# Optimization experiments

Hardware: AMD Instinct MI355X
Metric: run time of the kernel (lower is better)

## Reference

```python
import jax, jax.numpy as jnp
import numpy as np

B, D, H, FPL, L, LOG2_T = 65536, 768, 512, 4, 16, 19
T = 2 ** LOG2_T
BASE_RES, FINEST_RES = 16, 512
PRIMES = jnp.array([1, 2654435761, 805459861], dtype=jnp.uint32)


def setup_inputs() -> dict:
    key = jax.random.key(0)
    ks = jax.random.split(key, 8)
    t = jax.random.uniform(ks[0], (B,), dtype=jnp.float32)
    x = jax.random.normal(ks[1], (B, D), dtype=jnp.float32)
    cond = jax.random.uniform(ks[2], (B, 2), dtype=jnp.float32)
    # one embedding table per level, Instant-NGP init U(-1e-4, 1e-4)
    tables = jax.random.uniform(ks[3], (L, T, FPL), dtype=jnp.float32,
                                minval=-1e-4, maxval=1e-4)
    in_dim = D + L * FPL  # 832

    def lin(k, fan_in, fan_out):
        return jax.random.normal(k, (fan_in, fan_out), dtype=jnp.float32) / np.sqrt(fan_in).astype(np.float32)

    W0, b0 = lin(ks[4], in_dim, H), jnp.zeros((H,), jnp.float32)
    W1, b1 = lin(ks[5], H, H), jnp.zeros((H,), jnp.float32)
    W2, b2 = lin(ks[6], H, H), jnp.zeros((H,), jnp.float32)
    W3, b3 = lin(ks[7], H, D), jnp.zeros((D,), jnp.float32)
    return dict(t=t, x=x, cond=cond, tables=tables,
                W0=W0, b0=b0, W1=W1, b1=b1, W2=W2, b2=b2, W3=W3, b3=b3)


def hash_encode(coords, tables):
    """coords: [B,3] in [0,1]; tables: [L,T,F] -> [B, L*F]."""
    Ln, Tn, Fn = tables.shape
    growth = np.exp((np.log(FINEST_RES) - np.log(BASE_RES)) / (Ln - 1))
    scales = jnp.asarray(np.floor(BASE_RES * growth ** np.arange(Ln)),
                         dtype=coords.dtype)                      # [L]
    xf = coords[:, None, :] * scales[None, :, None]               # [B,L,3]
    xl = jnp.floor(xf)
    w = xf - xl                                                   # [B,L,3] trilinear frac
    xi = xl.astype(jnp.uint32)
    # 8 cube-corner offsets
    offs = jnp.asarray(np.stack(np.meshgrid([0, 1], [0, 1], [0, 1],
                                            indexing='ij'), -1).reshape(8, 3),
                       dtype=jnp.uint32)                          # [8,3]
    corners = xi[:, :, None, :] + offs[None, None]                # [B,L,8,3]
    h = corners * PRIMES                                          # uint32 wraparound hash
    idx = (h[..., 0] ^ h[..., 1] ^ h[..., 2]) & jnp.uint32(Tn - 1)  # [B,L,8]
    feats = tables[jnp.arange(Ln)[None, :, None], idx]            # [B,L,8,F] gather
    offs_f = offs.astype(coords.dtype)
    wc = jnp.prod(jnp.where(offs_f[None, None] == 1,
                            w[:, :, None, :], 1 - w[:, :, None, :]), axis=-1)  # [B,L,8]
    out = jnp.einsum('blc,blcf->blf', wc, feats)                  # [B,L,F]
    return out.reshape(out.shape[0], Ln * Fn)


def reference(t, x, cond, tables, W0, b0, W1, b1, W2, b2, W3, b3):
    tcol = t[:, None] if t.ndim == 1 else t
    params3 = jnp.concatenate([cond, tcol], axis=-1)   # [B,3]
    enc = hash_encode(params3, tables)                  # [B,64]
    h = jnp.concatenate([x, enc], axis=-1)              # [B,832]
    h = jax.nn.silu(h @ W0 + b0)
    h = jax.nn.silu(h @ W1 + b1)
    h = jax.nn.silu(h @ W2 + b2)
    return h @ W3 + b3                                  # [B,768]
```

## Files before the change

### kernel.cpp

```cpp
#include <hip/hip_runtime.h>
#include <hip/hip_bf16.h>
#include <math.h>


#define T_SIZE 524288
#define T_MASK (T_SIZE - 1)

typedef _Float16 f16;
typedef _Float16 f16x8 __attribute__((ext_vector_type(8)));
typedef _Float16 f16x4 __attribute__((ext_vector_type(4)));
typedef float f32x4 __attribute__((ext_vector_type(4)));

struct Scales { float s[16]; };

__global__ void wfrag(const float* __restrict__ W, f16* __restrict__ Wf, int K, int N) {
  int tid = blockIdx.x * 256 + threadIdx.x;
  int lane = tid & 63, frag = tid >> 6;
  int KS = K >> 5;
  int nblk = frag / KS, ks = frag - nblk * KS;
  if (nblk * 16 >= N) return;
  int n = nblk * 16 + (lane & 15);
  int kb = ks * 32 + (lane >> 4) * 8;
  f16x8 v;
#pragma unroll
  for (int j = 0; j < 8; ++j) v[j] = (f16)W[(size_t)(kb + j) * N + n];
  *(f16x8*)(Wf + (size_t)frag * 512 + lane * 8) = v;
}

__device__ __forceinline__ float silu_f(float v) {
  return v * __builtin_amdgcn_rcpf(1.f + __expf(-v));
}

__device__ __forceinline__ f16x8 cvt8(f32x4 a, f32x4 b) {
  return (f16x8){ (f16)a.x, (f16)a.y, (f16)a.z, (f16)a.w,
                  (f16)b.x, (f16)b.y, (f16)b.z, (f16)b.w };
}

template<int NF, int KSTEPS>
__device__ __forceinline__ void kloop_dp(
    const f16* __restrict__ actS, const f16* __restrict__ Wf, int fragRow0,
    int l16, int lhi, int lane, f32x4 (&acc)[4][4]) {
#pragma unroll
  for (int mi = 0; mi < 4; ++mi)
#pragma unroll
    for (int ni = 0; ni < NF; ++ni) acc[mi][ni] = (f32x4){0.f, 0.f, 0.f, 0.f};

  f16x8 bfU[NF], bfV[NF];
  const f16* wbase = Wf + ((size_t)fragRow0 * KSTEPS) * 512 + lane * 8;
#pragma unroll
  for (int ni = 0; ni < NF; ++ni)
    bfU[ni] = *(const f16x8*)(wbase + (size_t)(ni * KSTEPS + 0) * 512);
#pragma unroll
  for (int ni = 0; ni < NF; ++ni)
    bfV[ni] = *(const f16x8*)(wbase + (size_t)(ni * KSTEPS + 1) * 512);

#pragma unroll 1
  for (int ks = 0; ks < KSTEPS; ks += 2) {
    f16x8 af[4];
#pragma unroll
    for (int mi = 0; mi < 4; ++mi) {
      int r = mi * 16 + l16;
      af[mi] = *(const f16x8*)(actS + r * 512 + ((ks * 32 + lhi * 8) ^ ((r & 7) << 3)));
    }
#pragma unroll
    for (int mi = 0; mi < 4; ++mi)
#pragma unroll
      for (int ni = 0; ni < NF; ++ni)
        acc[mi][ni] = __builtin_amdgcn_mfma_f32_16x16x32_f16(bfU[ni], af[mi], acc[mi][ni], 0, 0, 0);
    if (ks + 2 < KSTEPS) {
#pragma unroll
      for (int ni = 0; ni < NF; ++ni)
        bfU[ni] = *(const f16x8*)(wbase + (size_t)(ni * KSTEPS + ks + 2) * 512);
    }
#pragma unroll
    for (int mi = 0; mi < 4; ++mi) {
      int r = mi * 16 + l16;
      af[mi] = *(const f16x8*)(actS + r * 512 + (((ks + 1) * 32 + lhi * 8) ^ ((r & 7) << 3)));
    }
#pragma unroll
    for (int mi = 0; mi < 4; ++mi)
#pragma unroll
      for (int ni = 0; ni < NF; ++ni)
        acc[mi][ni] = __builtin_amdgcn_mfma_f32_16x16x32_f16(bfV[ni], af[mi], acc[mi][ni], 0, 0, 0);
    if (ks + 3 < KSTEPS) {
#pragma unroll
      for (int ni = 0; ni < NF; ++ni)
        bfV[ni] = *(const f16x8*)(wbase + (size_t)(ni * KSTEPS + ks + 3) * 512);
    }
  }
}

__global__ __launch_bounds__(512, 4) void fused_mlp(
    const float* __restrict__ x, const float* __restrict__ t,
    const float* __restrict__ cond, const float* __restrict__ tables,
    const f16* __restrict__ Wf0, const f16* __restrict__ Wf1,
    const f16* __restrict__ Wf2, const f16* __restrict__ Wf3,
    const float* __restrict__ b0, const float* __restrict__ b1,
    const float* __restrict__ b2, const float* __restrict__ b3,
    float* __restrict__ outp, Scales scl) {
  __shared__ f16 act[64 * 512];
  f16* stg = act;
#define STG(p, kk) (stg + (p) * 5120 + (kk) * 2560)

  const int tid = threadIdx.x;
  const int wave = tid >> 6, lane = tid & 63;
  const int l16 = lane & 15, lhi = lane >> 4;
  const int rowBase = blockIdx.x * 64;
  const int sr = tid >> 3, c8 = tid & 7;
  const int skk = c8 >> 2, sco = (c8 & 3) * 8;

  f16x8 er;
  {
    int row = rowBase + sr;
    float c0 = cond[2 * row], c1 = cond[2 * row + 1], c2 = t[row];
    unsigned idx[2][8];
    float    wcw[2][8];
#pragma unroll
    for (int d = 0; d < 2; ++d) {
      int l = c8 * 2 + d;
      float s = scl.s[l];
      float xf0 = c0 * s, xf1 = c1 * s, xf2 = c2 * s;
      float xl0 = floorf(xf0), xl1 = floorf(xf1), xl2 = floorf(xf2);
      float w0 = xf0 - xl0, w1 = xf1 - xl1, w2 = xf2 - xl2;
      unsigned xi0 = (unsigned)xl0, xi1 = (unsigned)xl1, xi2 = (unsigned)xl2;
      unsigned h0 = xi0, h1 = xi1 * 2654435761u, h2 = xi2 * 805459861u;
      unsigned g0 = xi0 + 1u, g1 = (xi1 + 1u) * 2654435761u, g2 = (xi2 + 1u) * 805459861u;
#pragma unroll
      for (int c = 0; c < 8; ++c) {
        unsigned ax = (c >> 2) & 1u, ay = (c >> 1) & 1u, az = c & 1u;
        unsigned hh = (ax ? g0 : h0) ^ (ay ? g1 : h1) ^ (az ? g2 : h2);
        idx[d][c] = hh & T_MASK;
        wcw[d][c] = (ax ? w0 : 1.f - w0) * (ay ? w1 : 1.f - w1) * (az ? w2 : 1.f - w2);
      }
    }
    const f32x4* tl0 = (const f32x4*)tables + (size_t)(c8 * 2) * T_SIZE;
    f32x4 fv[2][8];
#pragma unroll
    for (int d = 0; d < 2; ++d)
#pragma unroll
      for (int c = 0; c < 8; ++c)
        fv[d][c] = tl0[(size_t)d * T_SIZE + idx[d][c]];
#pragma unroll
    for (int d = 0; d < 2; ++d) {
      float a0 = 0.f, a1 = 0.f, a2 = 0.f, a3 = 0.f;
#pragma unroll
      for (int c = 0; c < 8; ++c) {
        a0 += wcw[d][c] * fv[d][c].x; a1 += wcw[d][c] * fv[d][c].y;
        a2 += wcw[d][c] * fv[d][c].z; a3 += wcw[d][c] * fv[d][c].w;
      }
      er[d * 4 + 0] = (f16)a0; er[d * 4 + 1] = (f16)a1;
      er[d * 4 + 2] = (f16)a2; er[d * 4 + 3] = (f16)a3;
    }
  }

  f32x4 acc[4][4];
#pragma unroll
  for (int mi = 0; mi < 4; ++mi)
#pragma unroll
    for (int ni = 0; ni < 4; ++ni) acc[mi][ni] = (f32x4){0.f, 0.f, 0.f, 0.f};

  {
    const float* xrow = x + (size_t)(rowBase + sr) * 768 + c8 * 8;
    {
      f32x4 a = __builtin_nontemporal_load((const f32x4*)(xrow));
      f32x4 b = __builtin_nontemporal_load((const f32x4*)(xrow + 4));
      *(f16x8*)(STG(0, skk) + sr * 40 + sco) = cvt8(a, b);
    }
    f32x4 pA0 = __builtin_nontemporal_load((const f32x4*)(xrow + 64));
    f32x4 pA1 = __builtin_nontemporal_load((const f32x4*)(xrow + 68));
    f32x4 pB0, pB1;
    const f16* wb = Wf0 + lane * 8;
    __syncthreads();

#pragma unroll 1
    for (int ks = 0; ks < 13; ++ks) {
      if (ks + 2 < 12) {
        pB0 = __builtin_nontemporal_load((const f32x4*)(xrow + (ks + 2) * 64));
        pB1 = __builtin_nontemporal_load((const f32x4*)(xrow + (ks + 2) * 64 + 4));
      }
      f16x8 bf[2][4];
#pragma unroll
      for (int kk = 0; kk < 2; ++kk)
#pragma unroll
        for (int ni = 0; ni < 4; ++ni)
          bf[kk][ni] = *(const f16x8*)(wb + (size_t)((wave * 4 + ni) * 26 + 2 * ks + kk) * 512);

      const f16* rb = stg + (ks & 1) * 5120;
#pragma unroll
      for (int kk = 0; kk < 2; ++kk)
#pragma unroll
        for (int mi = 0; mi < 4; ++mi) {
          f16x8 af = *(const f16x8*)(rb + kk * 2560 + (mi * 16 + l16) * 40 + lhi * 8);
#pragma unroll
          for (int ni = 0; ni < 4; ++ni)
            acc[mi][ni] = __builtin_amdgcn_mfma_f32_16x16x32_f16(bf[kk][ni], af, acc[mi][ni], 0, 0, 0);
        }

      if (ks < 11) {
        *(f16x8*)(STG((ks + 1) & 1, skk) + sr * 40 + sco) = cvt8(pA0, pA1);
        pA0 = pB0; pA1 = pB1;
      } else if (ks == 11) {
        *(f16x8*)(STG(0, skk) + sr * 40 + sco) = er;
      }
      __syncthreads();
    }
  }

  auto epi_act = [&](const float* __restrict__ bias) {
    __syncthreads();
#pragma unroll
    for (int mi = 0; mi < 4; ++mi) {
      const int row = mi * 16 + l16;
#pragma unroll
      for (int ni = 0; ni < 4; ++ni) {
        const int col = wave * 64 + ni * 16 + lhi * 4;
        float4 bv = *(const float4*)(bias + col);
        f16x4 o;
        o[0] = (f16)silu_f(acc[mi][ni][0] + bv.x);
        o[1] = (f16)silu_f(acc[mi][ni][1] + bv.y);
        o[2] = (f16)silu_f(acc[mi][ni][2] + bv.z);
        o[3] = (f16)silu_f(acc[mi][ni][3] + bv.w);
        *(f16x4*)(act + row * 512 + (col ^ ((row & 7) << 3))) = o;
      }
    }
    __syncthreads();
  };
  epi_act(b0);

  kloop_dp<4, 16>(act, Wf1, wave * 4, l16, lhi, lane, acc); epi_act(b1);
  kloop_dp<4, 16>(act, Wf2, wave * 4, l16, lhi, lane, acc); epi_act(b2);

  kloop_dp<4, 16>(act, Wf3, wave * 4, l16, lhi, lane, acc);
#pragma unroll
  for (int mi = 0; mi < 4; ++mi) {
    const size_t row = (size_t)(rowBase + mi * 16 + l16);
#pragma unroll
    for (int ni = 0; ni < 4; ++ni) {
      const int col = wave * 64 + ni * 16 + lhi * 4;
      float4 bv = *(const float4*)(b3 + col);
      f32x4 o = { acc[mi][ni][0] + bv.x, acc[mi][ni][1] + bv.y,
                  acc[mi][ni][2] + bv.z, acc[mi][ni][3] + bv.w };
      __builtin_nontemporal_store(o, (f32x4*)(outp + row * 768 + col));
    }
  }

  kloop_dp<2, 16>(act, Wf3, 32 + wave * 2, l16, lhi, lane, acc);
#pragma unroll
  for (int mi = 0; mi < 4; ++mi) {
    const size_t row = (size_t)(rowBase + mi * 16 + l16);
#pragma unroll
    for (int ni = 0; ni < 2; ++ni) {
      const int col = 512 + wave * 32 + ni * 16 + lhi * 4;
      float4 bv = *(const float4*)(b3 + col);
      f32x4 o = { acc[mi][ni][0] + bv.x, acc[mi][ni][1] + bv.y,
                  acc[mi][ni][2] + bv.z, acc[mi][ni][3] + bv.w };
      __builtin_nontemporal_store(o, (f32x4*)(outp + row * 768 + col));
    }
  }
#undef STG
}

extern "C" void kernel_launch(void* const* d_in, const int* in_sizes, int n_in,
                              void* d_out, int out_size, void* d_ws, size_t ws_size,
                              hipStream_t stream) {
  const float* t    = (const float*)d_in[0];
  const float* x    = (const float*)d_in[1];
  const float* cond = (const float*)d_in[2];
  const float* tab  = (const float*)d_in[3];
  const float* W0   = (const float*)d_in[4];
  const float* b0   = (const float*)d_in[5];
  const float* W1   = (const float*)d_in[6];
  const float* b1   = (const float*)d_in[7];
  const float* W2   = (const float*)d_in[8];
  const float* b2   = (const float*)d_in[9];
  const float* W3   = (const float*)d_in[10];
  const float* b3   = (const float*)d_in[11];
  float* out = (float*)d_out;
  (void)in_sizes; (void)n_in; (void)out_size; (void)ws_size;

  char* ws = (char*)d_ws;
  f16* Wf0 = (f16*)(ws + 0);
  f16* Wf1 = (f16*)(ws + 851968);
  f16* Wf2 = (f16*)(ws + 1376256);
  f16* Wf3 = (f16*)(ws + 1900544);

  wfrag<<<dim3(208), 256, 0, stream>>>(W0, Wf0, 832, 512);
  wfrag<<<dim3(128), 256, 0, stream>>>(W1, Wf1, 512, 512);
  wfrag<<<dim3(128), 256, 0, stream>>>(W2, Wf2, 512, 512);
  wfrag<<<dim3(192), 256, 0, stream>>>(W3, Wf3, 512, 768);

  Scales sc;
  {
    double growth = exp((log(512.0) - log(16.0)) / 15.0);
    for (int l = 0; l < 16; ++l) sc.s[l] = (float)floor(16.0 * pow(growth, (double)l));
  }

  fused_mlp<<<dim3(1024), 512, 0, stream>>>(x, t, cond, tab, Wf0, Wf1, Wf2, Wf3,
                                            b0, b1, b2, b3, out, sc);
}
```

Before: 291.4 us.

## Split input prep into separate kernel and use 128-row blocks with direct LDS loads

Moves hash encoding and the fp32-to-fp16 conversion of x into a separate prep kernel that writes an f16 [B,832] buffer to workspace. The MLP kernel now uses 1024-thread blocks covering 128 rows, so each weight fragment loaded from global serves twice as many rows, and it streams layer-0 inputs with global_load_lds into swizzled double buffers. This adds an extra HBM round trip for the intermediate activations and a second launch, and a 128 KB LDS block limits occupancy to one block per CU.

```diff
diff --git a/kernel.cpp b/kernel.cpp
--- a/kernel.cpp
+++ b/kernel.cpp
@@ -12,6 +12,10 @@
 typedef float f32x4 __attribute__((ext_vector_type(4)));
 
 struct Scales { float s[16]; };
+
+#define GLD16(gsrc, ldst) __builtin_amdgcn_global_load_lds( \
+    (const __attribute__((address_space(1))) void*)(gsrc),  \
+    (__attribute__((address_space(3))) void*)(ldst), 16, 0, 0)
 
 __global__ void wfrag(const float* __restrict__ W, f16* __restrict__ Wf, int K, int N) {
   int tid = blockIdx.x * 256 + threadIdx.x;
@@ -36,82 +40,16 @@
                   (f16)b.x, (f16)b.y, (f16)b.z, (f16)b.w };
 }
 
-template<int NF, int KSTEPS>
-__device__ __forceinline__ void kloop_dp(
-    const f16* __restrict__ actS, const f16* __restrict__ Wf, int fragRow0,
-    int l16, int lhi, int lane, f32x4 (&acc)[4][4]) {
-#pragma unroll
-  for (int mi = 0; mi < 4; ++mi)
-#pragma unroll
-    for (int ni = 0; ni < NF; ++ni) acc[mi][ni] = (f32x4){0.f, 0.f, 0.f, 0.f};
-
-  f16x8 bfU[NF], bfV[NF];
-  const f16* wbase = Wf + ((size_t)fragRow0 * KSTEPS) * 512 + lane * 8;
-#pragma unroll
-  for (int ni = 0; ni < NF; ++ni)
-    bfU[ni] = *(const f16x8*)(wbase + (size_t)(ni * KSTEPS + 0) * 512);
-#pragma unroll
-  for (int ni = 0; ni < NF; ++ni)
-    bfV[ni] = *(const f16x8*)(wbase + (size_t)(ni * KSTEPS + 1) * 512);
-
-#pragma unroll 1
-  for (int ks = 0; ks < KSTEPS; ks += 2) {
-    f16x8 af[4];
-#pragma unroll
-    for (int mi = 0; mi < 4; ++mi) {
-      int r = mi * 16 + l16;
-      af[mi] = *(const f16x8*)(actS + r * 512 + ((ks * 32 + lhi * 8) ^ ((r & 7) << 3)));
-    }
-#pragma unroll
-    for (int mi = 0; mi < 4; ++mi)
-#pragma unroll
-      for (int ni = 0; ni < NF; ++ni)
-        acc[mi][ni] = __builtin_amdgcn_mfma_f32_16x16x32_f16(bfU[ni], af[mi], acc[mi][ni], 0, 0, 0);
-    if (ks + 2 < KSTEPS) {
-#pragma unroll
-      for (int ni = 0; ni < NF; ++ni)
-        bfU[ni] = *(const f16x8*)(wbase + (size_t)(ni * KSTEPS + ks + 2) * 512);
-    }
-#pragma unroll
-    for (int mi = 0; mi < 4; ++mi) {
-      int r = mi * 16 + l16;
-      af[mi] = *(const f16x8*)(actS + r * 512 + (((ks + 1) * 32 + lhi * 8) ^ ((r & 7) << 3)));
-    }
-#pragma unroll
-    for (int mi = 0; mi < 4; ++mi)
-#pragma unroll
-      for (int ni = 0; ni < NF; ++ni)
-        acc[mi][ni] = __builtin_amdgcn_mfma_f32_16x16x32_f16(bfV[ni], af[mi], acc[mi][ni], 0, 0, 0);
-    if (ks + 3 < KSTEPS) {
-#pragma unroll
-      for (int ni = 0; ni < NF; ++ni)
-        bfV[ni] = *(const f16x8*)(wbase + (size_t)(ni * KSTEPS + ks + 3) * 512);
-    }
-  }
-}
-
-__global__ __launch_bounds__(512, 4) void fused_mlp(
+__global__ __launch_bounds__(256) void prep(
     const float* __restrict__ x, const float* __restrict__ t,
     const float* __restrict__ cond, const float* __restrict__ tables,
-    const f16* __restrict__ Wf0, const f16* __restrict__ Wf1,
-    const f16* __restrict__ Wf2, const f16* __restrict__ Wf3,
-    const float* __restrict__ b0, const float* __restrict__ b1,
-    const float* __restrict__ b2, const float* __restrict__ b3,
-    float* __restrict__ outp, Scales scl) {
-  __shared__ f16 act[64 * 512];
-  f16* stg = act;
-#define STG(p, kk) (stg + (p) * 5120 + (kk) * 2560)
-
-  const int tid = threadIdx.x;
-  const int wave = tid >> 6, lane = tid & 63;
-  const int l16 = lane & 15, lhi = lane >> 4;
-  const int rowBase = blockIdx.x * 64;
-  const int sr = tid >> 3, c8 = tid & 7;
-  const int skk = c8 >> 2, sco = (c8 & 3) * 8;
-
-  f16x8 er;
+    f16* __restrict__ H0, Scales scl) {
+  const int row = blockIdx.x * 32 + (threadIdx.x >> 3);
+  const int c8 = threadIdx.x & 7;
+  const float* xr = x + (size_t)row * 768;
+  f16* hr = H0 + (size_t)row * 832;
+
   {
-    int row = rowBase + sr;
     float c0 = cond[2 * row], c1 = cond[2 * row + 1], c2 = t[row];
     unsigned idx[2][8];
     float    wcw[2][8];
@@ -140,6 +78,7 @@
 #pragma unroll
       for (int c = 0; c < 8; ++c)
         fv[d][c] = tl0[(size_t)d * T_SIZE + idx[d][c]];
+    f16x8 er;
 #pragma unroll
     for (int d = 0; d < 2; ++d) {
       float a0 = 0.f, a1 = 0.f, a2 = 0.f, a3 = 0.f;
@@ -151,7 +90,92 @@
       er[d * 4 + 0] = (f16)a0; er[d * 4 + 1] = (f16)a1;
       er[d * 4 + 2] = (f16)a2; er[d * 4 + 3] = (f16)a3;
     }
-  }
+    *(f16x8*)(hr + 768 + c8 * 8) = er;
+  }
+
+#pragma unroll
+  for (int j = 0; j < 12; ++j) {
+    int col = j * 64 + c8 * 8;
+    f32x4 a = __builtin_nontemporal_load((const f32x4*)(xr + col));
+    f32x4 b = __builtin_nontemporal_load((const f32x4*)(xr + col + 4));
+    *(f16x8*)(hr + col) = cvt8(a, b);
+  }
+}
+
+template<int NF, int KSTEPS>
+__device__ __forceinline__ void kloop_dp(
+    const f16* __restrict__ actS, const f16* __restrict__ Wf, int fragRow0,
+    int l16, int lhi, int lane, f32x4 (&acc)[4][4]) {
+#pragma unroll
+  for (int mi = 0; mi < 4; ++mi)
+#pragma unroll
+    for (int ni = 0; ni < NF; ++ni) acc[mi][ni] = (f32x4){0.f, 0.f, 0.f, 0.f};
+
+  f16x8 bfU[NF], bfV[NF];
+  const f16* wbase = Wf + ((size_t)fragRow0 * KSTEPS) * 512 + lane * 8;
+#pragma unroll
+  for (int ni = 0; ni < NF; ++ni)
+    bfU[ni] = *(const f16x8*)(wbase + (size_t)(ni * KSTEPS + 0) * 512);
+#pragma unroll
+  for (int ni = 0; ni < NF; ++ni)
+    bfV[ni] = *(const f16x8*)(wbase + (size_t)(ni * KSTEPS + 1) * 512);
+
+#pragma unroll 1
+  for (int ks = 0; ks < KSTEPS; ks += 2) {
+    f16x8 af[4];
+#pragma unroll
+    for (int mi = 0; mi < 4; ++mi) {
+      int r = mi * 16 + l16;
+      af[mi] = *(const f16x8*)(actS + r * 512 + ((ks * 32 + lhi * 8) ^ ((r & 7) << 3)));
+    }
+#pragma unroll
+    for (int mi = 0; mi < 4; ++mi)
+#pragma unroll
+      for (int ni = 0; ni < NF; ++ni)
+        acc[mi][ni] = __builtin_amdgcn_mfma_f32_16x16x32_f16(bfU[ni], af[mi], acc[mi][ni], 0, 0, 0);
+    if (ks + 2 < KSTEPS) {
+#pragma unroll
+      for (int ni = 0; ni < NF; ++ni)
+        bfU[ni] = *(const f16x8*)(wbase + (size_t)(ni * KSTEPS + ks + 2) * 512);
+    }
+#pragma unroll
+    for (int mi = 0; mi < 4; ++mi) {
+      int r = mi * 16 + l16;
+      af[mi] = *(const f16x8*)(actS + r * 512 + (((ks + 1) * 32 + lhi * 8) ^ ((r & 7) << 3)));
+    }
+#pragma unroll
+    for (int mi = 0; mi < 4; ++mi)
+#pragma unroll
+      for (int ni = 0; ni < NF; ++ni)
+        acc[mi][ni] = __builtin_amdgcn_mfma_f32_16x16x32_f16(bfV[ni], af[mi], acc[mi][ni], 0, 0, 0);
+    if (ks + 3 < KSTEPS) {
+#pragma unroll
+      for (int ni = 0; ni < NF; ++ni)
+        bfV[ni] = *(const f16x8*)(wbase + (size_t)(ni * KSTEPS + ks + 3) * 512);
+    }
+  }
+}
+
+__global__ __launch_bounds__(1024, 4) void fused_mlp(
+    const f16* __restrict__ H0,
+    const f16* __restrict__ Wf0, const f16* __restrict__ Wf1,
+    const f16* __restrict__ Wf2, const f16* __restrict__ Wf3,
+    const float* __restrict__ b0, const float* __restrict__ b1,
+    const float* __restrict__ b2, const float* __restrict__ b3,
+    float* __restrict__ outp) {
+  __shared__ f16 act[128 * 512];
+  f16* stg = act;
+
+  const int tid = threadIdx.x;
+  const int wave = tid >> 6, lane = tid & 63;
+  const int l16 = lane & 15, lhi = lane >> 4;
+  const int wr = wave >> 3, wc = wave & 7;
+  const int rowBase = blockIdx.x * 128;
+  const int r = tid >> 3, c8 = tid & 7;
+
+  const f16* h0r = H0 + (size_t)(rowBase + r) * 832 + (size_t)((c8 ^ (r & 7)) * 8);
+  f16* ldsA = stg + wave * 512;
+  f16* ldsB = stg + 8192 + wave * 512;
 
   f32x4 acc[4][4];
 #pragma unroll
@@ -160,48 +184,28 @@
     for (int ni = 0; ni < 4; ++ni) acc[mi][ni] = (f32x4){0.f, 0.f, 0.f, 0.f};
 
   {
-    const float* xrow = x + (size_t)(rowBase + sr) * 768 + c8 * 8;
-    {
-      f32x4 a = __builtin_nontemporal_load((const f32x4*)(xrow));
-      f32x4 b = __builtin_nontemporal_load((const f32x4*)(xrow + 4));
-      *(f16x8*)(STG(0, skk) + sr * 40 + sco) = cvt8(a, b);
-    }
-    f32x4 pA0 = __builtin_nontemporal_load((const f32x4*)(xrow + 64));
-    f32x4 pA1 = __builtin_nontemporal_load((const f32x4*)(xrow + 68));
-    f32x4 pB0, pB1;
-    const f16* wb = Wf0 + lane * 8;
+    GLD16(h0r, ldsA);
     __syncthreads();
-
 #pragma unroll 1
     for (int ks = 0; ks < 13; ++ks) {
-      if (ks + 2 < 12) {
-        pB0 = __builtin_nontemporal_load((const f32x4*)(xrow + (ks + 2) * 64));
-        pB1 = __builtin_nontemporal_load((const f32x4*)(xrow + (ks + 2) * 64 + 4));
-      }
+      if (ks < 12) GLD16(h0r + (ks + 1) * 64, (ks & 1) ? ldsA : ldsB);
       f16x8 bf[2][4];
 #pragma unroll
       for (int kk = 0; kk < 2; ++kk)
 #pragma unroll
         for (int ni = 0; ni < 4; ++ni)
-          bf[kk][ni] = *(const f16x8*)(wb + (size_t)((wave * 4 + ni) * 26 + 2 * ks + kk) * 512);
-
-      const f16* rb = stg + (ks & 1) * 5120;
+          bf[kk][ni] = *(const f16x8*)(Wf0 + (size_t)((wc * 4 + ni) * 26 + ks * 2 + kk) * 512 + lane * 8);
+      const f16* rb = stg + (ks & 1) * 8192 + wr * 4096;
 #pragma unroll
       for (int kk = 0; kk < 2; ++kk)
 #pragma unroll
         for (int mi = 0; mi < 4; ++mi) {
-          f16x8 af = *(const f16x8*)(rb + kk * 2560 + (mi * 16 + l16) * 40 + lhi * 8);
+          int r2 = mi * 16 + l16;
+          f16x8 af = *(const f16x8*)(rb + r2 * 64 + (((kk * 4 + lhi) ^ (r2 & 7)) << 3));
 #pragma unroll
           for (int ni = 0; ni < 4; ++ni)
             acc[mi][ni] = __builtin_amdgcn_mfma_f32_16x16x32_f16(bf[kk][ni], af, acc[mi][ni], 0, 0, 0);
         }
-
-      if (ks < 11) {
-        *(f16x8*)(STG((ks + 1) & 1, skk) + sr * 40 + sco) = cvt8(pA0, pA1);
-        pA0 = pB0; pA1 = pB1;
-      } else if (ks == 11) {
-        *(f16x8*)(STG(0, skk) + sr * 40 + sco) = er;
-      }
       __syncthreads();
     }
   }
@@ -210,10 +214,10 @@
     __syncthreads();
 #pragma unroll
     for (int mi = 0; mi < 4; ++mi) {
-      const int row = mi * 16 + l16;
+      const int row = wr * 64 + mi * 16 + l16;
 #pragma unroll
       for (int ni = 0; ni < 4; ++ni) {
-        const int col = wave * 64 + ni * 16 + lhi * 4;
+        const int col = wc * 64 + ni * 16 + lhi * 4;
         float4 bv = *(const float4*)(bias + col);
         f16x4 o;
         o[0] = (f16)silu_f(acc[mi][ni][0] + bv.x);
@@ -227,16 +231,18 @@
   };
   epi_act(b0);
 
-  kloop_dp<4, 16>(act, Wf1, wave * 4, l16, lhi, lane, acc); epi_act(b1);
-  kloop_dp<4, 16>(act, Wf2, wave * 4, l16, lhi, lane, acc); epi_act(b2);
-
-  kloop_dp<4, 16>(act, Wf3, wave * 4, l16, lhi, lane, acc);
+  const f16* actW = act + wr * 64 * 512;
+
+  kloop_dp<4, 16>(actW, Wf1, wc * 4, l16, lhi, lane, acc); epi_act(b1);
+  kloop_dp<4, 16>(actW, Wf2, wc * 4, l16, lhi, lane, acc); epi_act(b2);
+
+  kloop_dp<4, 16>(actW, Wf3, wc * 4, l16, lhi, lane, acc);
 #pragma unroll
   for (int mi = 0; mi < 4; ++mi) {
-    const size_t row = (size_t)(rowBase + mi * 16 + l16);
+    const size_t row = (size_t)(rowBase + wr * 64 + mi * 16 + l16);
 #pragma unroll
     for (int ni = 0; ni < 4; ++ni) {
-      const int col = wave * 64 + ni * 16 + lhi * 4;
+      const int col = wc * 64 + ni * 16 + lhi * 4;
       float4 bv = *(const float4*)(b3 + col);
       f32x4 o = { acc[mi][ni][0] + bv.x, acc[mi][ni][1] + bv.y,
                   acc[mi][ni][2] + bv.z, acc[mi][ni][3] + bv.w };
@@ -244,20 +250,19 @@
     }
   }
 
-  kloop_dp<2, 16>(act, Wf3, 32 + wave * 2, l16, lhi, lane, acc);
+  kloop_dp<2, 16>(actW, Wf3, 32 + wc * 2, l16, lhi, lane, acc);
 #pragma unroll
   for (int mi = 0; mi < 4; ++mi) {
-    const size_t row = (size_t)(rowBase + mi * 16 + l16);
+    const size_t row = (size_t)(rowBase + wr * 64 + mi * 16 + l16);
 #pragma unroll
     for (int ni = 0; ni < 2; ++ni) {
-      const int col = 512 + wave * 32 + ni * 16 + lhi * 4;
+      const int col = 512 + wc * 32 + ni * 16 + lhi * 4;
       float4 bv = *(const float4*)(b3 + col);
       f32x4 o = { acc[mi][ni][0] + bv.x, acc[mi][ni][1] + bv.y,
                   acc[mi][ni][2] + bv.z, acc[mi][ni][3] + bv.w };
       __builtin_nontemporal_store(o, (f32x4*)(outp + row * 768 + col));
     }
   }
-#undef STG
 }
 
 extern "C" void kernel_launch(void* const* d_in, const int* in_sizes, int n_in,
@@ -283,6 +288,7 @@
   f16* Wf1 = (f16*)(ws + 851968);
   f16* Wf2 = (f16*)(ws + 1376256);
   f16* Wf3 = (f16*)(ws + 1900544);
+  f16* H0  = (f16*)(ws + 2686976);
 
   wfrag<<<dim3(208), 256, 0, stream>>>(W0, Wf0, 832, 512);
   wfrag<<<dim3(128), 256, 0, stream>>>(W1, Wf1, 512, 512);
@@ -295,6 +301,8 @@
     for (int l = 0; l < 16; ++l) sc.s[l] = (float)floor(16.0 * pow(growth, (double)l));
   }
 
-  fused_mlp<<<dim3(1024), 512, 0, stream>>>(x, t, cond, tab, Wf0, Wf1, Wf2, Wf3,
-                                            b0, b1, b2, b3, out, sc);
-}
+  prep<<<dim3(2048), 256, 0, stream>>>(x, t, cond, tab, H0, sc);
+
+  fused_mlp<<<dim3(512), 1024, 0, stream>>>(H0, Wf0, Wf1, Wf2, Wf3,
+                                            b0, b1, b2, b3, out);
+}
```

Result: slower. 348.3 us (+19.5%).

## Stream x tiles into LDS via async global_load_lds with triple buffering

Applied to the files above, without the earlier changes.

Layer 0 now loads fp32 x tiles straight into LDS with global_load_lds (16-byte) into a triple-buffered, XOR-swizzled staging area, and converts to fp16 when reading the MFMA operands. The per-iteration __syncthreads is replaced by explicit vmcnt waits plus s_barrier, with raised wave priority around the MFMA block. The hash encoding result gets its own small LDS buffer and is consumed in a separate final k-step. The aim is to drop the register round-trip and the per-step store/sync for x staging and to overlap loads better. The cost is extra LDS (fp32 staging, more buffers), which may reduce occupancy, and it relies on hand-tuned waitcnt values.

```diff
diff --git a/kernel.cpp b/kernel.cpp
--- a/kernel.cpp
+++ b/kernel.cpp
@@ -12,6 +12,11 @@
 typedef float f32x4 __attribute__((ext_vector_type(4)));
 
 struct Scales { float s[16]; };
+
+#define GLD16(gsrc, ldst) __builtin_amdgcn_global_load_lds( \
+    (const __attribute__((address_space(1))) void*)(gsrc),  \
+    (__attribute__((address_space(3))) void*)(ldst), 16, 0, 0)
+#define SB() __builtin_amdgcn_sched_barrier(0)
 
 __global__ void wfrag(const float* __restrict__ W, f16* __restrict__ Wf, int K, int N) {
   int tid = blockIdx.x * 256 + threadIdx.x;
@@ -99,17 +104,15 @@
     const float* __restrict__ b2, const float* __restrict__ b3,
     float* __restrict__ outp, Scales scl) {
   __shared__ f16 act[64 * 512];
-  f16* stg = act;
-#define STG(p, kk) (stg + (p) * 5120 + (kk) * 2560)
+  __shared__ f16 encs[64 * 64];
+  char* stg = (char*)act;
 
   const int tid = threadIdx.x;
   const int wave = tid >> 6, lane = tid & 63;
   const int l16 = lane & 15, lhi = lane >> 4;
   const int rowBase = blockIdx.x * 64;
   const int sr = tid >> 3, c8 = tid & 7;
-  const int skk = c8 >> 2, sco = (c8 & 3) * 8;
-
-  f16x8 er;
+
   {
     int row = rowBase + sr;
     float c0 = cond[2 * row], c1 = cond[2 * row + 1], c2 = t[row];
@@ -140,6 +143,7 @@
 #pragma unroll
       for (int c = 0; c < 8; ++c)
         fv[d][c] = tl0[(size_t)d * T_SIZE + idx[d][c]];
+    f16x8 er;
 #pragma unroll
     for (int d = 0; d < 2; ++d) {
       float a0 = 0.f, a1 = 0.f, a2 = 0.f, a3 = 0.f;
@@ -151,6 +155,7 @@
       er[d * 4 + 0] = (f16)a0; er[d * 4 + 1] = (f16)a1;
       er[d * 4 + 2] = (f16)a2; er[d * 4 + 3] = (f16)a3;
     }
+    *(f16x8*)(encs + sr * 64 + ((c8 ^ (sr & 7)) * 8)) = er;
   }
 
   f32x4 acc[4][4];
@@ -160,49 +165,70 @@
     for (int ni = 0; ni < 4; ++ni) acc[mi][ni] = (f32x4){0.f, 0.f, 0.f, 0.f};
 
   {
-    const float* xrow = x + (size_t)(rowBase + sr) * 768 + c8 * 8;
-    {
-      f32x4 a = __builtin_nontemporal_load((const f32x4*)(xrow));
-      f32x4 b = __builtin_nontemporal_load((const f32x4*)(xrow + 4));
-      *(f16x8*)(STG(0, skk) + sr * 40 + sco) = cvt8(a, b);
-    }
-    f32x4 pA0 = __builtin_nontemporal_load((const f32x4*)(xrow + 64));
-    f32x4 pA1 = __builtin_nontemporal_load((const f32x4*)(xrow + 68));
-    f32x4 pB0, pB1;
-    const f16* wb = Wf0 + lane * 8;
+    const float* xsrc = x + (size_t)(rowBase + sr) * 768 + (size_t)((c8 ^ (sr & 7)) * 4);
+
+    GLD16(xsrc,      stg + wave * 1024);
+    GLD16(xsrc + 32, stg + 8192 + wave * 1024);
     __syncthreads();
 
+    int pr = 0, pw = 1;
 #pragma unroll 1
-    for (int ks = 0; ks < 13; ++ks) {
-      if (ks + 2 < 12) {
-        pB0 = __builtin_nontemporal_load((const f32x4*)(xrow + (ks + 2) * 64));
-        pB1 = __builtin_nontemporal_load((const f32x4*)(xrow + (ks + 2) * 64 + 4));
+    for (int s = 0; s < 12; ++s) {
+      if (s < 11) {
+        GLD16(xsrc + (s + 1) * 64,      stg + pw * 16384 + wave * 1024);
+        GLD16(xsrc + (s + 1) * 64 + 32, stg + pw * 16384 + 8192 + wave * 1024);
       }
+      SB();
       f16x8 bf[2][4];
 #pragma unroll
       for (int kk = 0; kk < 2; ++kk)
 #pragma unroll
         for (int ni = 0; ni < 4; ++ni)
-          bf[kk][ni] = *(const f16x8*)(wb + (size_t)((wave * 4 + ni) * 26 + 2 * ks + kk) * 512);
-
-      const f16* rb = stg + (ks & 1) * 5120;
+          bf[kk][ni] = *(const f16x8*)(Wf0 + (size_t)((wave * 4 + ni) * 26 + 2 * s + kk) * 512 + lane * 8);
+      SB();
+      if (s < 11) asm volatile("s_waitcnt vmcnt(10)" ::: "memory");
+      else        asm volatile("s_waitcnt vmcnt(8)"  ::: "memory");
+      SB();
+      __builtin_amdgcn_s_barrier();
+      SB();
+      const char* rb = stg + pr * 16384;
+      __builtin_amdgcn_s_setprio(1);
 #pragma unroll
       for (int kk = 0; kk < 2; ++kk)
 #pragma unroll
         for (int mi = 0; mi < 4; ++mi) {
-          f16x8 af = *(const f16x8*)(rb + kk * 2560 + (mi * 16 + l16) * 40 + lhi * 8);
+          int r2 = mi * 16 + l16;
+          const char* rowb = rb + kk * 8192 + r2 * 128;
+          f32x4 a = *(const f32x4*)(rowb + (((lhi * 2)     ^ (r2 & 7)) << 4));
+          f32x4 b = *(const f32x4*)(rowb + (((lhi * 2 + 1) ^ (r2 & 7)) << 4));
+          f16x8 af = cvt8(a, b);
 #pragma unroll
           for (int ni = 0; ni < 4; ++ni)
             acc[mi][ni] = __builtin_amdgcn_mfma_f32_16x16x32_f16(bf[kk][ni], af, acc[mi][ni], 0, 0, 0);
         }
-
-      if (ks < 11) {
-        *(f16x8*)(STG((ks + 1) & 1, skk) + sr * 40 + sco) = cvt8(pA0, pA1);
-        pA0 = pB0; pA1 = pB1;
-      } else if (ks == 11) {
-        *(f16x8*)(STG(0, skk) + sr * 40 + sco) = er;
-      }
-      __syncthreads();
+      __builtin_amdgcn_s_setprio(0);
+      SB();
+      pr = (pr == 2) ? 0 : pr + 1;
+      pw = (pw == 2) ? 0 : pw + 1;
+    }
+
+    {
+      f16x8 bf[2][4];
+#pragma unroll
+      for (int kk = 0; kk < 2; ++kk)
+#pragma unroll
+        for (int ni = 0; ni < 4; ++ni)
+          bf[kk][ni] = *(const f16x8*)(Wf0 + (size_t)((wave * 4 + ni) * 26 + 24 + kk) * 512 + lane * 8);
+#pragma unroll
+      for (int kk = 0; kk < 2; ++kk)
+#pragma unroll
+        for (int mi = 0; mi < 4; ++mi) {
+          int r2 = mi * 16 + l16;
+          f16x8 af = *(const f16x8*)(encs + r2 * 64 + (((kk * 4 + lhi) ^ (r2 & 7)) * 8));
+#pragma unroll
+          for (int ni = 0; ni < 4; ++ni)
+            acc[mi][ni] = __builtin_amdgcn_mfma_f32_16x16x32_f16(bf[kk][ni], af, acc[mi][ni], 0, 0, 0);
+        }
     }
   }
 
@@ -257,7 +283,6 @@
       __builtin_nontemporal_store(o, (f32x4*)(outp + row * 768 + col));
     }
   }
-#undef STG
 }
 
 extern "C" void kernel_launch(void* const* d_in, const int* in_sizes, int n_in,
```

Result: slower. 299.2 us (+2.7%).

## Split hash encoding and x conversion into a prep kernel writing MFMA fragments

Applied to the files above, without the earlier changes.

Moves the hash-grid encoding and the fp32-to-fp16 conversion of x out of the fused MLP into a separate prep kernel. That kernel writes the layer-0 input directly in MFMA fragment layout to workspace. The first layer then reads A fragments straight from global memory with register double-buffering, with no LDS staging or per-step barriers. The cost is an extra kernel launch and a round trip of about 109 MB of fp16 activations through HBM, in exchange for removing the gather latency and barriers from the MLP kernel.

```diff
diff --git a/kernel.cpp b/kernel.cpp
--- a/kernel.cpp
+++ b/kernel.cpp
@@ -36,88 +36,33 @@
                   (f16)b.x, (f16)b.y, (f16)b.z, (f16)b.w };
 }
 
-template<int NF, int KSTEPS>
-__device__ __forceinline__ void kloop_dp(
-    const f16* __restrict__ actS, const f16* __restrict__ Wf, int fragRow0,
-    int l16, int lhi, int lane, f32x4 (&acc)[4][4]) {
-#pragma unroll
-  for (int mi = 0; mi < 4; ++mi)
-#pragma unroll
-    for (int ni = 0; ni < NF; ++ni) acc[mi][ni] = (f32x4){0.f, 0.f, 0.f, 0.f};
-
-  f16x8 bfU[NF], bfV[NF];
-  const f16* wbase = Wf + ((size_t)fragRow0 * KSTEPS) * 512 + lane * 8;
-#pragma unroll
-  for (int ni = 0; ni < NF; ++ni)
-    bfU[ni] = *(const f16x8*)(wbase + (size_t)(ni * KSTEPS + 0) * 512);
-#pragma unroll
-  for (int ni = 0; ni < NF; ++ni)
-    bfV[ni] = *(const f16x8*)(wbase + (size_t)(ni * KSTEPS + 1) * 512);
-
-#pragma unroll 1
-  for (int ks = 0; ks < KSTEPS; ks += 2) {
-    f16x8 af[4];
-#pragma unroll
-    for (int mi = 0; mi < 4; ++mi) {
-      int r = mi * 16 + l16;
-      af[mi] = *(const f16x8*)(actS + r * 512 + ((ks * 32 + lhi * 8) ^ ((r & 7) << 3)));
-    }
-#pragma unroll
-    for (int mi = 0; mi < 4; ++mi)
-#pragma unroll
-      for (int ni = 0; ni < NF; ++ni)
-        acc[mi][ni] = __builtin_amdgcn_mfma_f32_16x16x32_f16(bfU[ni], af[mi], acc[mi][ni], 0, 0, 0);
-    if (ks + 2 < KSTEPS) {
-#pragma unroll
-      for (int ni = 0; ni < NF; ++ni)
-        bfU[ni] = *(const f16x8*)(wbase + (size_t)(ni * KSTEPS + ks + 2) * 512);
-    }
-#pragma unroll
-    for (int mi = 0; mi < 4; ++mi) {
-      int r = mi * 16 + l16;
-      af[mi] = *(const f16x8*)(actS + r * 512 + (((ks + 1) * 32 + lhi * 8) ^ ((r & 7) << 3)));
-    }
-#pragma unroll
-    for (int mi = 0; mi < 4; ++mi)
-#pragma unroll
-      for (int ni = 0; ni < NF; ++ni)
-        acc[mi][ni] = __builtin_amdgcn_mfma_f32_16x16x32_f16(bfV[ni], af[mi], acc[mi][ni], 0, 0, 0);
-    if (ks + 3 < KSTEPS) {
-#pragma unroll
-      for (int ni = 0; ni < NF; ++ni)
-        bfV[ni] = *(const f16x8*)(wbase + (size_t)(ni * KSTEPS + ks + 3) * 512);
-    }
-  }
-}
-
-__global__ __launch_bounds__(512, 4) void fused_mlp(
+__global__ __launch_bounds__(256) void prep(
     const float* __restrict__ x, const float* __restrict__ t,
     const float* __restrict__ cond, const float* __restrict__ tables,
-    const f16* __restrict__ Wf0, const f16* __restrict__ Wf1,
-    const f16* __restrict__ Wf2, const f16* __restrict__ Wf3,
-    const float* __restrict__ b0, const float* __restrict__ b1,
-    const float* __restrict__ b2, const float* __restrict__ b3,
-    float* __restrict__ outp, Scales scl) {
-  __shared__ f16 act[64 * 512];
-  f16* stg = act;
-#define STG(p, kk) (stg + (p) * 5120 + (kk) * 2560)
-
-  const int tid = threadIdx.x;
-  const int wave = tid >> 6, lane = tid & 63;
+    f16* __restrict__ H0f, Scales scl) {
+  const int blk = blockIdx.x;
+  const int wave = threadIdx.x >> 6, lane = threadIdx.x & 63;
   const int l16 = lane & 15, lhi = lane >> 4;
-  const int rowBase = blockIdx.x * 64;
-  const int sr = tid >> 3, c8 = tid & 7;
-  const int skk = c8 >> 2, sco = (c8 & 3) * 8;
-
-  f16x8 er;
-  {
-    int row = rowBase + sr;
-    float c0 = cond[2 * row], c1 = cond[2 * row + 1], c2 = t[row];
+  const int mi = wave;
+  const int row = blk * 64 + mi * 16 + l16;
+  const float* xr = x + (size_t)row * 768 + lhi * 8;
+  f16* fb = H0f + ((size_t)blk * 104 + mi) * 512 + lane * 8;
+
+#pragma unroll 4
+  for (int ks = 0; ks < 24; ++ks) {
+    f32x4 a = __builtin_nontemporal_load((const f32x4*)(xr + ks * 32));
+    f32x4 b = __builtin_nontemporal_load((const f32x4*)(xr + ks * 32 + 4));
+    *(f16x8*)(fb + (size_t)ks * 2048) = cvt8(a, b);
+  }
+
+  const float c0 = cond[2 * row], c1 = cond[2 * row + 1], c2 = t[row];
+#pragma unroll
+  for (int e = 0; e < 2; ++e) {
     unsigned idx[2][8];
     float    wcw[2][8];
 #pragma unroll
     for (int d = 0; d < 2; ++d) {
-      int l = c8 * 2 + d;
+      int l = e * 8 + lhi * 2 + d;
       float s = scl.s[l];
       float xf0 = c0 * s, xf1 = c1 * s, xf2 = c2 * s;
       float xl0 = floorf(xf0), xl1 = floorf(xf1), xl2 = floorf(xf2);
@@ -133,13 +78,14 @@
         wcw[d][c] = (ax ? w0 : 1.f - w0) * (ay ? w1 : 1.f - w1) * (az ? w2 : 1.f - w2);
       }
     }
-    const f32x4* tl0 = (const f32x4*)tables + (size_t)(c8 * 2) * T_SIZE;
     f32x4 fv[2][8];
 #pragma unroll
-    for (int d = 0; d < 2; ++d)
-#pragma unroll
-      for (int c = 0; c < 8; ++c)
-        fv[d][c] = tl0[(size_t)d * T_SIZE + idx[d][c]];
+    for (int d = 0; d < 2; ++d) {
+      const f32x4* tl = (const f32x4*)tables + (size_t)(e * 8 + lhi * 2 + d) * T_SIZE;
+#pragma unroll
+      for (int c = 0; c < 8; ++c) fv[d][c] = tl[idx[d][c]];
+    }
+    f16x8 er;
 #pragma unroll
     for (int d = 0; d < 2; ++d) {
       float a0 = 0.f, a1 = 0.f, a2 = 0.f, a3 = 0.f;
@@ -151,7 +97,77 @@
       er[d * 4 + 0] = (f16)a0; er[d * 4 + 1] = (f16)a1;
       er[d * 4 + 2] = (f16)a2; er[d * 4 + 3] = (f16)a3;
     }
-  }
+    *(f16x8*)(fb + (size_t)(24 + e) * 2048) = er;
+  }
+}
+
+template<int NF, int KSTEPS>
+__device__ __forceinline__ void kloop_dp(
+    const f16* __restrict__ actS, const f16* __restrict__ Wf, int fragRow0,
+    int l16, int lhi, int lane, f32x4 (&acc)[4][4]) {
+#pragma unroll
+  for (int mi = 0; mi < 4; ++mi)
+#pragma unroll
+    for (int ni = 0; ni < NF; ++ni) acc[mi][ni] = (f32x4){0.f, 0.f, 0.f, 0.f};
+
+  f16x8 bfU[NF], bfV[NF];
+  const f16* wbase = Wf + ((size_t)fragRow0 * KSTEPS) * 512 + lane * 8;
+#pragma unroll
+  for (int ni = 0; ni < NF; ++ni)
+    bfU[ni] = *(const f16x8*)(wbase + (size_t)(ni * KSTEPS + 0) * 512);
+#pragma unroll
+  for (int ni = 0; ni < NF; ++ni)
+    bfV[ni] = *(const f16x8*)(wbase + (size_t)(ni * KSTEPS + 1) * 512);
+
+#pragma unroll 1
+  for (int ks = 0; ks < KSTEPS; ks += 2) {
+    f16x8 af[4];
+#pragma unroll
+    for (int mi = 0; mi < 4; ++mi) {
+      int r = mi * 16 + l16;
+      af[mi] = *(const f16x8*)(actS + r * 512 + ((ks * 32 + lhi * 8) ^ ((r & 7) << 3)));
+    }
+#pragma unroll
+    for (int mi = 0; mi < 4; ++mi)
+#pragma unroll
+      for (int ni = 0; ni < NF; ++ni)
+        acc[mi][ni] = __builtin_amdgcn_mfma_f32_16x16x32_f16(bfU[ni], af[mi], acc[mi][ni], 0, 0, 0);
+    if (ks + 2 < KSTEPS) {
+#pragma unroll
+      for (int ni = 0; ni < NF; ++ni)
+        bfU[ni] = *(const f16x8*)(wbase + (size_t)(ni * KSTEPS + ks + 2) * 512);
+    }
+#pragma unroll
+    for (int mi = 0; mi < 4; ++mi) {
+      int r = mi * 16 + l16;
+      af[mi] = *(const f16x8*)(actS + r * 512 + (((ks + 1) * 32 + lhi * 8) ^ ((r & 7) << 3)));
+    }
+#pragma unroll
+    for (int mi = 0; mi < 4; ++mi)
+#pragma unroll
+      for (int ni = 0; ni < NF; ++ni)
+        acc[mi][ni] = __builtin_amdgcn_mfma_f32_16x16x32_f16(bfV[ni], af[mi], acc[mi][ni], 0, 0, 0);
+    if (ks + 3 < KSTEPS) {
+#pragma unroll
+      for (int ni = 0; ni < NF; ++ni)
+        bfV[ni] = *(const f16x8*)(wbase + (size_t)(ni * KSTEPS + ks + 3) * 512);
+    }
+  }
+}
+
+__global__ __launch_bounds__(512, 4) void fused_mlp(
+    const f16* __restrict__ H0f,
+    const f16* __restrict__ Wf0, const f16* __restrict__ Wf1,
+    const f16* __restrict__ Wf2, const f16* __restrict__ Wf3,
+    const float* __restrict__ b0, const float* __restrict__ b1,
+    const float* __restrict__ b2, const float* __restrict__ b3,
+    float* __restrict__ outp) {
+  __shared__ f16 act[64 * 512];
+
+  const int tid = threadIdx.x;
+  const int wave = tid >> 6, lane = tid & 63;
+  const int l16 = lane & 15, lhi = lane >> 4;
+  const int rowBase = blockIdx.x * 64;
 
   f32x4 acc[4][4];
 #pragma unroll
@@ -160,49 +176,48 @@
     for (int ni = 0; ni < 4; ++ni) acc[mi][ni] = (f32x4){0.f, 0.f, 0.f, 0.f};
 
   {
-    const float* xrow = x + (size_t)(rowBase + sr) * 768 + c8 * 8;
-    {
-      f32x4 a = __builtin_nontemporal_load((const f32x4*)(xrow));
-      f32x4 b = __builtin_nontemporal_load((const f32x4*)(xrow + 4));
-      *(f16x8*)(STG(0, skk) + sr * 40 + sco) = cvt8(a, b);
-    }
-    f32x4 pA0 = __builtin_nontemporal_load((const f32x4*)(xrow + 64));
-    f32x4 pA1 = __builtin_nontemporal_load((const f32x4*)(xrow + 68));
-    f32x4 pB0, pB1;
+    const f16* fb = H0f + (size_t)blockIdx.x * 104 * 512 + lane * 8;
     const f16* wb = Wf0 + lane * 8;
-    __syncthreads();
+    f16x8 afU[4], afV[4], bfU[4], bfV[4];
+#pragma unroll
+    for (int mi = 0; mi < 4; ++mi) afU[mi] = *(const f16x8*)(fb + (size_t)(0 * 4 + mi) * 512);
+#pragma unroll
+    for (int ni = 0; ni < 4; ++ni)
+      bfU[ni] = *(const f16x8*)(wb + (size_t)((wave * 4 + ni) * 26 + 0) * 512);
+#pragma unroll
+    for (int mi = 0; mi < 4; ++mi) afV[mi] = *(const f16x8*)(fb + (size_t)(1 * 4 + mi) * 512);
+#pragma unroll
+    for (int ni = 0; ni < 4; ++ni)
+      bfV[ni] = *(const f16x8*)(wb + (size_t)((wave * 4 + ni) * 26 + 1) * 512);
 
 #pragma unroll 1
-    for (int ks = 0; ks < 13; ++ks) {
-      if (ks + 2 < 12) {
-        pB0 = __builtin_nontemporal_load((const f32x4*)(xrow + (ks + 2) * 64));
-        pB1 = __builtin_nontemporal_load((const f32x4*)(xrow + (ks + 2) * 64 + 4));
-      }
-      f16x8 bf[2][4];
-#pragma unroll
-      for (int kk = 0; kk < 2; ++kk)
+    for (int ks = 0; ks < 26; ks += 2) {
+#pragma unroll
+      for (int mi = 0; mi < 4; ++mi)
 #pragma unroll
         for (int ni = 0; ni < 4; ++ni)
-          bf[kk][ni] = *(const f16x8*)(wb + (size_t)((wave * 4 + ni) * 26 + 2 * ks + kk) * 512);
-
-      const f16* rb = stg + (ks & 1) * 5120;
-#pragma unroll
-      for (int kk = 0; kk < 2; ++kk)
-#pragma unroll
-        for (int mi = 0; mi < 4; ++mi) {
-          f16x8 af = *(const f16x8*)(rb + kk * 2560 + (mi * 16 + l16) * 40 + lhi * 8);
-#pragma unroll
-          for (int ni = 0; ni < 4; ++ni)
-            acc[mi][ni] = __builtin_amdgcn_mfma_f32_16x16x32_f16(bf[kk][ni], af, acc[mi][ni], 0, 0, 0);
-        }
-
-      if (ks < 11) {
-        *(f16x8*)(STG((ks + 1) & 1, skk) + sr * 40 + sco) = cvt8(pA0, pA1);
-        pA0 = pB0; pA1 = pB1;
-      } else if (ks == 11) {
-        *(f16x8*)(STG(0, skk) + sr * 40 + sco) = er;
-      }
-      __syncthreads();
+          acc[mi][ni] = __builtin_amdgcn_mfma_f32_16x16x32_f16(bfU[ni], afU[mi], acc[mi][ni], 0, 0, 0);
+      if (ks + 2 < 26) {
+#pragma unroll
+        for (int mi = 0; mi < 4; ++mi)
+          afU[mi] = *(const f16x8*)(fb + (size_t)((ks + 2) * 4 + mi) * 512);
+#pragma unroll
+        for (int ni = 0; ni < 4; ++ni)
+          bfU[ni] = *(const f16x8*)(wb + (size_t)((wave * 4 + ni) * 26 + ks + 2) * 512);
+      }
+#pragma unroll
+      for (int mi = 0; mi < 4; ++mi)
+#pragma unroll
+        for (int ni = 0; ni < 4; ++ni)
+          acc[mi][ni] = __builtin_amdgcn_mfma_f32_16x16x32_f16(bfV[ni], afV[mi], acc[mi][ni], 0, 0, 0);
+      if (ks + 3 < 26) {
+#pragma unroll
+        for (int mi = 0; mi < 4; ++mi)
+          afV[mi] = *(const f16x8*)(fb + (size_t)((ks + 3) * 4 + mi) * 512);
+#pragma unroll
+        for (int ni = 0; ni < 4; ++ni)
+          bfV[ni] = *(const f16x8*)(wb + (size_t)((wave * 4 + ni) * 26 + ks + 3) * 512);
+      }
     }
   }
 
@@ -257,7 +272,6 @@
       __builtin_nontemporal_store(o, (f32x4*)(outp + row * 768 + col));
     }
   }
-#undef STG
 }
 
 extern "C" void kernel_launch(void* const* d_in, const int* in_sizes, int n_in,
@@ -283,6 +297,7 @@
   f16* Wf1 = (f16*)(ws + 851968);
   f16* Wf2 = (f16*)(ws + 1376256);
   f16* Wf3 = (f16*)(ws + 1900544);
+  f16* H0f = (f16*)(ws + 2686976);
 
   wfrag<<<dim3(208), 256, 0, stream>>>(W0, Wf0, 832, 512);
   wfrag<<<dim3(128), 256, 0, stream>>>(W1, Wf1, 512, 512);
@@ -295,6 +310,8 @@
     for (int l = 0; l < 16; ++l) sc.s[l] = (float)floor(16.0 * pow(growth, (double)l));
   }
 
-  fused_mlp<<<dim3(1024), 512, 0, stream>>>(x, t, cond, tab, Wf0, Wf1, Wf2, Wf3,
-                                            b0, b1, b2, b3, out, sc);
-}
+  prep<<<dim3(1024), 256, 0, stream>>>(x, t, cond, tab, H0f, sc);
+
+  fused_mlp<<<dim3(1024), 512, 0, stream>>>(H0f, Wf0, Wf1, Wf2, Wf3,
+                                            b0, b1, b2, b3, out);
+}
```

After: 388.7 us. 1.33x slower.
